# Optimization experiments

Hardware: AMD Instinct MI355X
Metric: run time of the kernel (lower is better)

Reference implementation:

```python
import jax, jax.numpy as jnp
import numpy as np

N = 100000      # num_nodes
E = 400000      # num edges
HID = 128       # hidden_channels (== in_channels, memory dim)
OUT = 64        # out_channels (per head)
HEADS = 4
HD = HEADS * OUT  # 256, TransformerConv concat output dim


def _lin(k, fan_in, fan_out):
    return jax.random.normal(k, (fan_in, fan_out), jnp.float32) * 0.02


def setup_inputs() -> dict:
    key = jax.random.key(0)
    ks = jax.random.split(key, 16)
    return {
        "edge_index": jax.random.randint(ks[0], (2, E), 0, N, dtype=jnp.int64),
        "edge_time": jax.random.randint(ks[1], (E, 1), 0, 1000000, dtype=jnp.int64),
        "x": jax.random.normal(ks[2], (N, HID), jnp.float32),
        "memory": jax.random.normal(ks[3], (N, HID), jnp.float32),  # TGN memory table (detached in fwd)
        # TransformerConv params (lin_query / lin_key / lin_value / lin_skip, all with bias)
        "Wq": _lin(ks[4], HID, HD), "bq": jnp.zeros((HD,), jnp.float32),
        "Wk": _lin(ks[5], HID, HD), "bk": jnp.zeros((HD,), jnp.float32),
        "Wv": _lin(ks[6], HID, HD), "bv": jnp.zeros((HD,), jnp.float32),
        "Wskip": _lin(ks[7], HID, HD), "bskip": jnp.zeros((HD,), jnp.float32),
        # rating MLP: Linear(512,128) -> ReLU -> Linear(128,64) -> ReLU -> Linear(64,1)
        "W1": _lin(ks[8], 2 * HD, 128), "b1": jnp.zeros((128,), jnp.float32),
        "W2": _lin(ks[9], 128, 64), "b2": jnp.zeros((64,), jnp.float32),
        "W3": _lin(ks[10], 64, 1), "b3": jnp.zeros((1,), jnp.float32),
    }


def reference(edge_index, edge_time, x, memory,
              Wq, bq, Wk, bk, Wv, bv, Wskip, bskip,
              W1, b1, W2, b2, W3, b3):
    src, dst = edge_index[0], edge_index[1]
    n = x.shape[0]

    # x = memory.detach() + x
    h = memory + x  # [N, HID]

    # TransformerConv (heads=4, concat=True, root_weight=True)
    q = (h @ Wq + bq).reshape(n, HEADS, OUT)
    k = (h @ Wk + bk).reshape(n, HEADS, OUT)
    v = (h @ Wv + bv).reshape(n, HEADS, OUT)

    # per-edge attention scores: messages flow src -> dst, softmax over in-edges of dst
    scores = jnp.sum(q[dst] * k[src], axis=-1) / jnp.sqrt(jnp.float32(OUT))  # [E, H]
    smax = jax.ops.segment_max(scores, dst, num_segments=n)                   # [N, H]
    e = jnp.exp(scores - smax[dst])
    denom = jax.ops.segment_sum(e, dst, num_segments=n)
    alpha = e / (denom[dst] + 1e-16)                                          # [E, H]

    agg = jax.ops.segment_sum(alpha[:, :, None] * v[src], dst, num_segments=n)  # [N, H, OUT]
    out = agg.reshape(n, HD) + (h @ Wskip + bskip)                              # skip connection

    # interaction embeddings + MLP head (dropout inactive at eval)
    inter = jnp.concatenate([out[src], out[dst]], axis=-1)  # [E, 512]
    hdd = jax.nn.relu(inter @ W1 + b1)
    hdd = jax.nn.relu(hdd @ W2 + b2)
    rating = jax.nn.sigmoid(hdd @ W3 + b3) * 4.0 + 1.0
    return rating[:, 0]
```

## Files before the change

kernel.cpp:

```cpp
#include <hip/hip_runtime.h>
#include <math.h>

#define N_NODES 100000
#define N_EDGES 400000
#define HID 128
#define HEADS 4
#define OUT_C 64
#define HD 256
#define SCAN_CHUNK 1024
#define NB_SCAN ((N_NODES + SCAN_CHUNK - 1) / SCAN_CHUNK)

typedef __attribute__((ext_vector_type(8))) short bf16x8;
typedef __attribute__((ext_vector_type(4))) float f32x4;

__device__ __forceinline__ unsigned short fbf(float f) {
    unsigned u = __float_as_uint(f);
    unsigned r = (u + 0x7fffu + ((u >> 16) & 1u)) >> 16;
    return (unsigned short)r;
}
__device__ __forceinline__ float bf2f(unsigned short u) {
    return __uint_as_float(((unsigned)u) << 16);
}

__global__ __launch_bounds__(256) void init_zero(int* __restrict__ deg,
                                                 int* __restrict__ cursor) {
    int i = blockIdx.x * 256 + threadIdx.x;
    if (i < N_NODES) { deg[i] = 0; cursor[i] = 0; }
}

__global__ __launch_bounds__(256) void k_deg(const int* __restrict__ ei,
                                             int* __restrict__ deg) {
    int e = blockIdx.x * 256 + threadIdx.x;
    if (e < N_EDGES) atomicAdd(&deg[ei[N_EDGES + e]], 1);
}

__global__ __launch_bounds__(256) void k_scan1(const int* __restrict__ deg,
                                               int* __restrict__ rp,
                                               int* __restrict__ bsum) {
    __shared__ int ts[256];
    int b = blockIdx.x, t = threadIdx.x;
    int base = b * SCAN_CHUNK + t * 4;
    int vv[4];
    int s = 0;
#pragma unroll
    for (int i = 0; i < 4; ++i) {
        int d = (base + i < N_NODES) ? deg[base + i] : 0;
        vv[i] = s;
        s += d;
    }
    ts[t] = s;
    __syncthreads();
    for (int off = 1; off < 256; off <<= 1) {
        int x = (t >= off) ? ts[t - off] : 0;
        __syncthreads();
        ts[t] += x;
        __syncthreads();
    }
    int ex = ts[t] - s;
#pragma unroll
    for (int i = 0; i < 4; ++i)
        if (base + i < N_NODES) rp[base + i] = ex + vv[i];
    if (t == 255) bsum[b] = ts[255];
}

__global__ __launch_bounds__(256) void k_scan2(int* __restrict__ bsum) {
    __shared__ int ts[256];
    int t = threadIdx.x;
    int v = (t < NB_SCAN) ? bsum[t] : 0;
    ts[t] = v;
    __syncthreads();
    for (int off = 1; off < 256; off <<= 1) {
        int x = (t >= off) ? ts[t - off] : 0;
        __syncthreads();
        ts[t] += x;
        __syncthreads();
    }
    if (t < NB_SCAN) bsum[t] = ts[t] - v;
}

__global__ __launch_bounds__(256) void k_scan3(int* __restrict__ rp,
                                               const int* __restrict__ bsum) {
    int i = blockIdx.x * 256 + threadIdx.x;
    if (i < N_NODES) rp[i] += bsum[i / SCAN_CHUNK];
}

__global__ __launch_bounds__(256) void k_bucket(const int* __restrict__ ei,
                                                const int* __restrict__ rp,
                                                int* __restrict__ cursor,
                                                int* __restrict__ csr_src,
                                                int* __restrict__ csr_dst,
                                                int* __restrict__ csr_eid) {
    int e = blockIdx.x * 256 + threadIdx.x;
    if (e >= N_EDGES) return;
    int src = ei[e];
    int d   = ei[N_EDGES + e];
    int idx = atomicAdd(&cursor[d], 1);
    int s   = rp[d] + idx;
    csr_src[s] = src;
    csr_dst[s] = d;
    csr_eid[s] = e;
}

__global__ __launch_bounds__(256) void pack_wg(
    const float* __restrict__ Wq, const float* __restrict__ Wk,
    const float* __restrict__ Wv, const float* __restrict__ Ws,
    unsigned short* __restrict__ Wp) {
    int i = blockIdx.x * 256 + threadIdx.x;
    if (i >= 16384) return;
    int lane = i & 63, nt = (i >> 6) & 15, kt = (i >> 10) & 3, z = i >> 12;
    const float* W = (z == 0) ? Wq : (z == 1) ? Wk : (z == 2) ? Wv : Ws;
    int q = lane >> 4, c = lane & 15;
#pragma unroll
    for (int j = 0; j < 8; ++j)
        Wp[i * 8 + j] = fbf(W[(kt * 32 + q * 8 + j) * HD + nt * 16 + c]);
}

__global__ __launch_bounds__(256) void pack_wc(const float* __restrict__ W1,
                                               unsigned short* __restrict__ Wcp) {
    int i = blockIdx.x * 256 + threadIdx.x;
    if (i >= 8192) return;
    int lane = i & 63, nt = (i >> 6) & 15, kt = i >> 10;
    int q = lane >> 4, c = lane & 15;
    int n = nt * 16 + c;
#pragma unroll
    for (int j = 0; j < 8; ++j) {
        int k = kt * 32 + q * 8 + j;
        float v = (n < 128) ? W1[k * 128 + n] : W1[(k + 256) * 128 + (n - 128)];
        Wcp[i * 8 + j] = fbf(v);
    }
}

__global__ __launch_bounds__(256) void pack_w2(const float* __restrict__ W2,
                                               unsigned short* __restrict__ W2p) {
    int i = blockIdx.x * 256 + threadIdx.x;
    if (i >= 1024) return;
    int lane = i & 63, nt = (i >> 6) & 3, kt = i >> 8;
    int q = lane >> 4, c = lane & 15;
#pragma unroll
    for (int j = 0; j < 8; ++j)
        W2p[i * 8 + j] = fbf(W2[(kt * 32 + q * 8 + j) * 64 + nt * 16 + c]);
}

__global__ __launch_bounds__(256) void gemm_proj(
    const float* __restrict__ x, const float* __restrict__ mem,
    const unsigned short* __restrict__ Wp,
    const float* __restrict__ bq, const float* __restrict__ bk,
    const float* __restrict__ bv, const float* __restrict__ bs,
    unsigned short* __restrict__ Q, unsigned short* __restrict__ K,
    unsigned short* __restrict__ V, unsigned short* __restrict__ S)
{
    __shared__ __align__(16) short As[64 * 136];
    __shared__ __align__(16) short Slab[4 * 64 * 68];

    const int t = threadIdx.x;
    const int w = t >> 6, l = t & 63;
    const int q = l >> 4, c = l & 15;
    const int m0 = blockIdx.x * 64;

    {
        const float4* x4 = (const float4*)x;
        const float4* m4 = (const float4*)mem;
#pragma unroll
        for (int j = 0; j < 8; ++j) {
            int idx = t + j * 256;
            int row = idx >> 5, c4 = idx & 31;
            int gr  = m0 + row;
            ushort4 hv = make_ushort4(0, 0, 0, 0);
            if (gr < N_NODES) {
                float4 a = x4[(size_t)gr * 32 + c4];
                float4 b = m4[(size_t)gr * 32 + c4];
                hv = make_ushort4(fbf(a.x + b.x), fbf(a.y + b.y),
                                  fbf(a.z + b.z), fbf(a.w + b.w));
            }
            *(ushort4*)&As[row * 136 + c4 * 4] = hv;
        }
    }
    __syncthreads();

    short* slab = &Slab[w * 64 * 68];
    const int srow = l >> 3;
    const int schk = l & 7;

    for (int z = 0; z < 4; ++z) {
        const float* bz = (z == 0) ? bq : (z == 1) ? bk : (z == 2) ? bv : bs;
        unsigned short* Oz = (z == 0) ? Q : (z == 1) ? K : (z == 2) ? V : S;

        f32x4 acc[4][4];
#pragma unroll
        for (int mt = 0; mt < 4; ++mt)
#pragma unroll
            for (int nt = 0; nt < 4; ++nt) acc[mt][nt] = (f32x4){0.f, 0.f, 0.f, 0.f};

#pragma unroll
        for (int kt = 0; kt < 4; ++kt) {
            bf16x8 af[4];
#pragma unroll
            for (int mt = 0; mt < 4; ++mt)
                af[mt] = *(const bf16x8*)&As[(mt * 16 + c) * 136 + kt * 32 + q * 8];
#pragma unroll
            for (int nt = 0; nt < 4; ++nt) {
                int ntg = w * 4 + nt;
                bf16x8 bv8 = *(const bf16x8*)&Wp[(size_t)(((z * 4 + kt) * 16 + ntg) * 64 + l) * 8];
#pragma unroll
                for (int mt = 0; mt < 4; ++mt)
                    acc[mt][nt] = __builtin_amdgcn_mfma_f32_16x16x32_bf16(af[mt], bv8, acc[mt][nt], 0, 0, 0);
            }
        }

#pragma unroll
        for (int nt = 0; nt < 4; ++nt) {
            float bb = bz[w * 64 + nt * 16 + c];
#pragma unroll
            for (int mt = 0; mt < 4; ++mt)
#pragma unroll
                for (int r = 0; r < 4; ++r)
                    slab[(mt * 16 + q * 4 + r) * 68 + nt * 16 + c] =
                        (short)fbf(acc[mt][nt][r] + bb);
        }
#pragma unroll
        for (int j = 0; j < 8; ++j) {
            int row = j * 8 + srow;
            int gr = m0 + row;
            if (gr < N_NODES)
                *(bf16x8*)&Oz[(size_t)gr * HD + w * 64 + schk * 8] =
                    *(const bf16x8*)&slab[row * 68 + schk * 8];
        }
    }
}

__global__ __launch_bounds__(256) void k_attn(
    const int* __restrict__ rp, const int* __restrict__ deg,
    const int* __restrict__ csr_src,
    const unsigned short* __restrict__ Q, const unsigned short* __restrict__ K,
    const unsigned short* __restrict__ V, const unsigned short* __restrict__ S,
    unsigned short* __restrict__ out)
{
    int node = blockIdx.x * 4 + (threadIdx.x >> 6);
    int l = threadIdx.x & 63;
    if (node >= N_NODES) return;
    int start = rp[node];
    int cnt   = deg[node];

    float q0, q1, q2, q3;
    {
        ushort4 u = *(const ushort4*)&Q[(size_t)node * HD + l * 4];
        q0 = bf2f(u.x); q1 = bf2f(u.y); q2 = bf2f(u.z); q3 = bf2f(u.w);
    }

    float m = -1e30f, d = 0.f;
    float a0 = 0.f, a1 = 0.f, a2 = 0.f, a3 = 0.f;

    for (int i = 0; i < cnt; ++i) {
        int src = csr_src[start + i];
        ushort4 ku = *(const ushort4*)&K[(size_t)src * HD + l * 4];
        float s = q0 * bf2f(ku.x) + q1 * bf2f(ku.y) + q2 * bf2f(ku.z) + q3 * bf2f(ku.w);
        s += __shfl_xor(s, 1);
        s += __shfl_xor(s, 2);
        s += __shfl_xor(s, 4);
        s += __shfl_xor(s, 8);
        s *= 0.125f;

        float mn    = fmaxf(m, s);
        float scale = __expf(m - mn);
        float e     = __expf(s - mn);
        d = d * scale + e;
        ushort4 vu = *(const ushort4*)&V[(size_t)src * HD + l * 4];
        a0 = a0 * scale + e * bf2f(vu.x);
        a1 = a1 * scale + e * bf2f(vu.y);
        a2 = a2 * scale + e * bf2f(vu.z);
        a3 = a3 * scale + e * bf2f(vu.w);
        m = mn;
    }

    float inv = 1.f / (d + 1e-16f);
    ushort4 su = *(const ushort4*)&S[(size_t)node * HD + l * 4];
    ushort4 ov = make_ushort4(fbf(bf2f(su.x) + a0 * inv),
                              fbf(bf2f(su.y) + a1 * inv),
                              fbf(bf2f(su.z) + a2 * inv),
                              fbf(bf2f(su.w) + a3 * inv));
    *(ushort4*)&out[(size_t)node * HD + l * 4] = ov;
}

__global__ __launch_bounds__(256) void pd_gemm(
    const unsigned short* __restrict__ outb,
    const unsigned short* __restrict__ Wcp,
    unsigned short* __restrict__ PD)
{
    __shared__ __align__(16) char sh[4 * 64 * 68 * 2];
    short* As   = (short*)sh;
    short* Slab = (short*)sh;

    const int t = threadIdx.x;
    const int w = t >> 6, l = t & 63;
    const int q = l >> 4, c = l & 15;
    const int m0 = blockIdx.x * 64;

#pragma unroll
    for (int j = 0; j < 8; ++j) {
        int idx = t + j * 256;
        int row = idx >> 5, c4 = idx & 31;
        int gr  = m0 + row;
        bf16x8 v = (bf16x8){0,0,0,0,0,0,0,0};
        if (gr < N_NODES)
            v = *(const bf16x8*)&outb[(size_t)gr * HD + c4 * 8];
        *(bf16x8*)&As[row * 264 + c4 * 8] = v;
    }
    __syncthreads();

    f32x4 acc[4][4];
#pragma unroll
    for (int mt = 0; mt < 4; ++mt)
#pragma unroll
        for (int nt = 0; nt < 4; ++nt) acc[mt][nt] = (f32x4){0.f, 0.f, 0.f, 0.f};

#pragma unroll
    for (int kt = 0; kt < 8; ++kt) {
        bf16x8 af[4];
#pragma unroll
        for (int mt = 0; mt < 4; ++mt)
            af[mt] = *(const bf16x8*)&As[(mt * 16 + c) * 264 + kt * 32 + q * 8];
#pragma unroll
        for (int nt = 0; nt < 4; ++nt) {
            int ntg = w * 4 + nt;
            bf16x8 bv8 = *(const bf16x8*)&Wcp[(size_t)((kt * 16 + ntg) * 64 + l) * 8];
#pragma unroll
            for (int mt = 0; mt < 4; ++mt)
                acc[mt][nt] = __builtin_amdgcn_mfma_f32_16x16x32_bf16(af[mt], bv8, acc[mt][nt], 0, 0, 0);
        }
    }
    __syncthreads();

    short* slab = &Slab[w * 64 * 68];
#pragma unroll
    for (int nt = 0; nt < 4; ++nt)
#pragma unroll
        for (int mt = 0; mt < 4; ++mt)
#pragma unroll
            for (int r = 0; r < 4; ++r)
                slab[(mt * 16 + q * 4 + r) * 68 + nt * 16 + c] =
                    (short)fbf(acc[mt][nt][r]);
    const int srow = l >> 3, schk = l & 7;
#pragma unroll
    for (int j = 0; j < 8; ++j) {
        int row = j * 8 + srow;
        int gr = m0 + row;
        if (gr < N_NODES)
            *(bf16x8*)&PD[(size_t)gr * HD + w * 64 + schk * 8] =
                *(const bf16x8*)&slab[row * 68 + schk * 8];
    }
}

__global__ __launch_bounds__(256) void edge_mlp_pd(
    const int* __restrict__ csr_src, const int* __restrict__ csr_dst,
    const int* __restrict__ csr_eid,
    const unsigned short* __restrict__ PD,
    const float* __restrict__ b1,
    const unsigned short* __restrict__ W2p, const float* __restrict__ b2,
    const float* __restrict__ W3, const float* __restrict__ b3,
    float* __restrict__ rating)
{
    __shared__ __align__(16) char lds[64 * 136 * 2];
    short* h1t = (short*)lds;
    float* h2s = (float*)lds;

    const int t = threadIdx.x;
    const int w = t >> 6, l = t & 63;
    const int q = l >> 4, c = l & 15;
    const int e0 = blockIdx.x * 64;

#pragma unroll
    for (int j = 0; j < 4; ++j) {
        int idx = t + j * 256;
        int row = idx >> 4, ch = idx & 15;
        int src = csr_src[e0 + row];
        int dst = csr_dst[e0 + row];
        bf16x8 pv = *(const bf16x8*)&PD[(size_t)src * HD + ch * 8];
        bf16x8 dv = *(const bf16x8*)&PD[(size_t)dst * HD + 128 + ch * 8];
        float4 ba = *(const float4*)&b1[ch * 8];
        float4 bb = *(const float4*)&b1[ch * 8 + 4];
        bf16x8 hv;
        hv[0] = (short)fbf(fmaxf(bf2f((unsigned short)pv[0]) + bf2f((unsigned short)dv[0]) + ba.x, 0.f));
        hv[1] = (short)fbf(fmaxf(bf2f((unsigned short)pv[1]) + bf2f((unsigned short)dv[1]) + ba.y, 0.f));
        hv[2] = (short)fbf(fmaxf(bf2f((unsigned short)pv[2]) + bf2f((unsigned short)dv[2]) + ba.z, 0.f));
        hv[3] = (short)fbf(fmaxf(bf2f((unsigned short)pv[3]) + bf2f((unsigned short)dv[3]) + ba.w, 0.f));
        hv[4] = (short)fbf(fmaxf(bf2f((unsigned short)pv[4]) + bf2f((unsigned short)dv[4]) + bb.x, 0.f));
        hv[5] = (short)fbf(fmaxf(bf2f((unsigned short)pv[5]) + bf2f((unsigned short)dv[5]) + bb.y, 0.f));
        hv[6] = (short)fbf(fmaxf(bf2f((unsigned short)pv[6]) + bf2f((unsigned short)dv[6]) + bb.z, 0.f));
        hv[7] = (short)fbf(fmaxf(bf2f((unsigned short)pv[7]) + bf2f((unsigned short)dv[7]) + bb.w, 0.f));
        *(bf16x8*)&h1t[row * 136 + ch * 8] = hv;
    }
    __syncthreads();

    f32x4 acc2[4];
#pragma unroll
    for (int i = 0; i < 4; ++i) acc2[i] = (f32x4){0.f, 0.f, 0.f, 0.f};
#pragma unroll
    for (int kt = 0; kt < 4; ++kt) {
        bf16x8 av = *(const bf16x8*)&h1t[(w * 16 + c) * 136 + kt * 32 + q * 8];
#pragma unroll
        for (int nt = 0; nt < 4; ++nt) {
            bf16x8 bv = *(const bf16x8*)&W2p[(size_t)((kt * 4 + nt) * 64 + l) * 8];
            acc2[nt] = __builtin_amdgcn_mfma_f32_16x16x32_bf16(av, bv, acc2[nt], 0, 0, 0);
        }
    }
    __syncthreads();

#pragma unroll
    for (int nt = 0; nt < 4; ++nt) {
        float bv = b2[nt * 16 + c];
#pragma unroll
        for (int r = 0; r < 4; ++r)
            h2s[(w * 16 + q * 4 + r) * 65 + nt * 16 + c] = fmaxf(acc2[nt][r] + bv, 0.f);
    }
    __syncthreads();

    if (t < 64) {
        float a = b3[0];
#pragma unroll 8
        for (int kk = 0; kk < 64; ++kk)
            a += h2s[t * 65 + kk] * W3[kk];
        rating[csr_eid[e0 + t]] = 4.f / (1.f + __expf(-a)) + 1.f;
    }
}

extern "C" void kernel_launch(void* const* d_in, const int* in_sizes, int n_in,
                              void* d_out, int out_size, void* d_ws, size_t ws_size,
                              hipStream_t stream) {
    const int*   ei  = (const int*)d_in[0];
    const float* x   = (const float*)d_in[2];
    const float* mem = (const float*)d_in[3];
    const float* Wq  = (const float*)d_in[4];
    const float* bq  = (const float*)d_in[5];
    const float* Wk  = (const float*)d_in[6];
    const float* bk  = (const float*)d_in[7];
    const float* Wv  = (const float*)d_in[8];
    const float* bv  = (const float*)d_in[9];
    const float* Ws  = (const float*)d_in[10];
    const float* bs  = (const float*)d_in[11];
    const float* W1  = (const float*)d_in[12];
    const float* b1  = (const float*)d_in[13];
    const float* W2  = (const float*)d_in[14];
    const float* b2  = (const float*)d_in[15];
    const float* W3  = (const float*)d_in[16];
    const float* b3  = (const float*)d_in[17];
    float* rating = (float*)d_out;

    unsigned short* Q = (unsigned short*)d_ws;
    const size_t NHDe = (size_t)N_NODES * HD;
    unsigned short* K = Q + NHDe;
    unsigned short* V = K + NHDe;
    unsigned short* S = V + NHDe;
    int* rp      = (int*)(S + NHDe);
    int* deg     = rp + N_NODES;
    int* cursor  = deg + N_NODES;
    int* csr_src = cursor + N_NODES;
    int* csr_dst = csr_src + N_EDGES;
    int* csr_eid = csr_dst + N_EDGES;
    int* bsum    = csr_eid + N_EDGES;
    unsigned short* Wp  = (unsigned short*)(bsum + 128);
    unsigned short* Wcp = Wp + 16384 * 8;
    unsigned short* W2p = Wcp + 8192 * 8;
    unsigned short* PD  = K;

    const int nblk  = (N_NODES + 255) / 256;
    const int eblk  = (N_EDGES + 255) / 256;
    const int wgrid = (N_NODES + 3) / 4;

    init_zero<<<nblk, 256, 0, stream>>>(deg, cursor);
    k_deg<<<eblk, 256, 0, stream>>>(ei, deg);
    k_scan1<<<NB_SCAN, 256, 0, stream>>>(deg, rp, bsum);
    k_scan2<<<1, 256, 0, stream>>>(bsum);
    k_scan3<<<nblk, 256, 0, stream>>>(rp, bsum);
    k_bucket<<<eblk, 256, 0, stream>>>(ei, rp, cursor, csr_src, csr_dst, csr_eid);
    pack_wg<<<64, 256, 0, stream>>>(Wq, Wk, Wv, Ws, Wp);
    pack_wc<<<32, 256, 0, stream>>>(W1, Wcp);
    pack_w2<<<4, 256, 0, stream>>>(W2, W2p);

    gemm_proj<<<(N_NODES + 63) / 64, 256, 0, stream>>>(
        x, mem, Wp, bq, bk, bv, bs, Q, K, V, S);

    k_attn<<<wgrid, 256, 0, stream>>>(rp, deg, csr_src, Q, K, V, S, Q);

    pd_gemm<<<(N_NODES + 63) / 64, 256, 0, stream>>>(Q, Wcp, PD);

    edge_mlp_pd<<<N_EDGES / 64, 256, 0, stream>>>(
        csr_src, csr_dst, csr_eid, PD, b1, W2p, b2, W3, b3, rating);
}
```

Before: 500.3 us.

## Interleave K and V rows, split projection GEMM over grid, precompute bf16 H

Adds a pre-pass that converts memory+x to a bf16 H table. The projection GEMM is split across a 2D grid with one output matrix per blockIdx.y, and it loads H tiles straight into LDS with XOR-swizzled global_load_lds. K and V are stored interleaved in one 512-wide row, so the attention gather fetches both from the same row region. This buys more parallelism and better locality for the per-edge gather. The cost is an extra kernel launch, an extra round trip of H through memory, and each A tile being reloaded four times.

```diff
diff --git a/kernel.cpp b/kernel.cpp
--- a/kernel.cpp
+++ b/kernel.cpp
@@ -20,6 +20,13 @@
 }
 __device__ __forceinline__ float bf2f(unsigned short u) {
     return __uint_as_float(((unsigned)u) << 16);
+}
+
+__device__ __forceinline__ void gl_lds16(const void* g, void* l) {
+    __builtin_amdgcn_global_load_lds(
+        (const __attribute__((address_space(1))) unsigned int*)g,
+        (__attribute__((address_space(3))) unsigned int*)l,
+        16, 0, 0);
 }
 
 __global__ __launch_bounds__(256) void init_zero(int* __restrict__ deg,
@@ -141,98 +148,111 @@
         W2p[i * 8 + j] = fbf(W2[(kt * 32 + q * 8 + j) * 64 + nt * 16 + c]);
 }
 
-__global__ __launch_bounds__(256) void gemm_proj(
-    const float* __restrict__ x, const float* __restrict__ mem,
+__global__ __launch_bounds__(256) void k_pre(const float* __restrict__ x,
+                                             const float* __restrict__ mem,
+                                             unsigned short* __restrict__ H) {
+    int idx = blockIdx.x * 256 + threadIdx.x;
+    if (idx >= N_NODES * HID / 8) return;
+    const float4* x4 = (const float4*)x;
+    const float4* m4 = (const float4*)mem;
+    float4 a0 = x4[(size_t)idx * 2],     a1 = x4[(size_t)idx * 2 + 1];
+    float4 b0 = m4[(size_t)idx * 2],     b1 = m4[(size_t)idx * 2 + 1];
+    bf16x8 hv;
+    hv[0] = (short)fbf(a0.x + b0.x); hv[1] = (short)fbf(a0.y + b0.y);
+    hv[2] = (short)fbf(a0.z + b0.z); hv[3] = (short)fbf(a0.w + b0.w);
+    hv[4] = (short)fbf(a1.x + b1.x); hv[5] = (short)fbf(a1.y + b1.y);
+    hv[6] = (short)fbf(a1.z + b1.z); hv[7] = (short)fbf(a1.w + b1.w);
+    *(bf16x8*)&H[(size_t)idx * 8] = hv;
+}
+
+__global__ __launch_bounds__(256, 4) void gemm4(
+    const unsigned short* __restrict__ H,
     const unsigned short* __restrict__ Wp,
     const float* __restrict__ bq, const float* __restrict__ bk,
     const float* __restrict__ bv, const float* __restrict__ bs,
-    unsigned short* __restrict__ Q, unsigned short* __restrict__ K,
-    unsigned short* __restrict__ V, unsigned short* __restrict__ S)
+    unsigned short* __restrict__ Q, unsigned short* __restrict__ KV,
+    unsigned short* __restrict__ S)
 {
-    __shared__ __align__(16) short As[64 * 136];
-    __shared__ __align__(16) short Slab[4 * 64 * 68];
+    __shared__ __align__(16) short sh[4 * 64 * 68];
+    short* As = sh;
 
     const int t = threadIdx.x;
     const int w = t >> 6, l = t & 63;
     const int q = l >> 4, c = l & 15;
+    const int z  = blockIdx.y;
     const int m0 = blockIdx.x * 64;
 
-    {
-        const float4* x4 = (const float4*)x;
-        const float4* m4 = (const float4*)mem;
-#pragma unroll
-        for (int j = 0; j < 8; ++j) {
-            int idx = t + j * 256;
-            int row = idx >> 5, c4 = idx & 31;
-            int gr  = m0 + row;
-            ushort4 hv = make_ushort4(0, 0, 0, 0);
-            if (gr < N_NODES) {
-                float4 a = x4[(size_t)gr * 32 + c4];
-                float4 b = m4[(size_t)gr * 32 + c4];
-                hv = make_ushort4(fbf(a.x + b.x), fbf(a.y + b.y),
-                                  fbf(a.z + b.z), fbf(a.w + b.w));
-            }
-            *(ushort4*)&As[row * 136 + c4 * 4] = hv;
+#pragma unroll
+    for (int i = 0; i < 4; ++i) {
+        int rbase = w * 16 + i * 4;
+        int r  = rbase + (l >> 4);
+        int gr = m0 + r; if (gr >= N_NODES) gr = N_NODES - 1;
+        int ks = (l & 15) ^ (r & 7);
+        gl_lds16(&H[(size_t)gr * HID + ks * 8], &As[rbase * 128]);
+    }
+
+    unsigned short* Oz; int rs, coff; const float* bz;
+    if      (z == 0) { Oz = Q;  rs = 256; coff = 0;   bz = bq; }
+    else if (z == 1) { Oz = KV; rs = 512; coff = 0;   bz = bk; }
+    else if (z == 2) { Oz = KV; rs = 512; coff = 256; bz = bv; }
+    else             { Oz = S;  rs = 256; coff = 0;   bz = bs; }
+    float bb[4];
+#pragma unroll
+    for (int nt = 0; nt < 4; ++nt) bb[nt] = bz[w * 64 + nt * 16 + c];
+
+    f32x4 acc[4][4];
+#pragma unroll
+    for (int mt = 0; mt < 4; ++mt)
+#pragma unroll
+        for (int nt = 0; nt < 4; ++nt) acc[mt][nt] = (f32x4){0.f, 0.f, 0.f, 0.f};
+
+    __syncthreads();
+
+#pragma unroll
+    for (int kt = 0; kt < 4; ++kt) {
+        bf16x8 af[4];
+#pragma unroll
+        for (int mt = 0; mt < 4; ++mt) {
+            int row  = mt * 16 + c;
+            int slot = (kt * 4 + q) ^ (row & 7);
+            af[mt] = *(const bf16x8*)&As[row * 128 + slot * 8];
         }
-    }
-    __syncthreads();
-
-    short* slab = &Slab[w * 64 * 68];
-    const int srow = l >> 3;
-    const int schk = l & 7;
-
-    for (int z = 0; z < 4; ++z) {
-        const float* bz = (z == 0) ? bq : (z == 1) ? bk : (z == 2) ? bv : bs;
-        unsigned short* Oz = (z == 0) ? Q : (z == 1) ? K : (z == 2) ? V : S;
-
-        f32x4 acc[4][4];
+#pragma unroll
+        for (int nt = 0; nt < 4; ++nt) {
+            bf16x8 bw8 = *(const bf16x8*)&Wp[(size_t)(((z * 4 + kt) * 16 + w * 4 + nt) * 64 + l) * 8];
+#pragma unroll
+            for (int mt = 0; mt < 4; ++mt)
+                acc[mt][nt] = __builtin_amdgcn_mfma_f32_16x16x32_bf16(af[mt], bw8, acc[mt][nt], 0, 0, 0);
+        }
+    }
+    __syncthreads();
+
+    short* slab = &sh[w * 64 * 68];
+#pragma unroll
+    for (int nt = 0; nt < 4; ++nt)
 #pragma unroll
         for (int mt = 0; mt < 4; ++mt)
 #pragma unroll
-            for (int nt = 0; nt < 4; ++nt) acc[mt][nt] = (f32x4){0.f, 0.f, 0.f, 0.f};
-
-#pragma unroll
-        for (int kt = 0; kt < 4; ++kt) {
-            bf16x8 af[4];
-#pragma unroll
-            for (int mt = 0; mt < 4; ++mt)
-                af[mt] = *(const bf16x8*)&As[(mt * 16 + c) * 136 + kt * 32 + q * 8];
-#pragma unroll
-            for (int nt = 0; nt < 4; ++nt) {
-                int ntg = w * 4 + nt;
-                bf16x8 bv8 = *(const bf16x8*)&Wp[(size_t)(((z * 4 + kt) * 16 + ntg) * 64 + l) * 8];
-#pragma unroll
-                for (int mt = 0; mt < 4; ++mt)
-                    acc[mt][nt] = __builtin_amdgcn_mfma_f32_16x16x32_bf16(af[mt], bv8, acc[mt][nt], 0, 0, 0);
-            }
-        }
-
-#pragma unroll
-        for (int nt = 0; nt < 4; ++nt) {
-            float bb = bz[w * 64 + nt * 16 + c];
-#pragma unroll
-            for (int mt = 0; mt < 4; ++mt)
-#pragma unroll
-                for (int r = 0; r < 4; ++r)
-                    slab[(mt * 16 + q * 4 + r) * 68 + nt * 16 + c] =
-                        (short)fbf(acc[mt][nt][r] + bb);
-        }
-#pragma unroll
-        for (int j = 0; j < 8; ++j) {
-            int row = j * 8 + srow;
-            int gr = m0 + row;
-            if (gr < N_NODES)
-                *(bf16x8*)&Oz[(size_t)gr * HD + w * 64 + schk * 8] =
-                    *(const bf16x8*)&slab[row * 68 + schk * 8];
-        }
+            for (int r = 0; r < 4; ++r)
+                slab[(mt * 16 + q * 4 + r) * 68 + nt * 16 + c] =
+                    (short)fbf(acc[mt][nt][r] + bb[nt]);
+
+    const int srow = l >> 3, schk = l & 7;
+#pragma unroll
+    for (int j = 0; j < 8; ++j) {
+        int row = j * 8 + srow;
+        int gr  = m0 + row;
+        if (gr < N_NODES)
+            *(bf16x8*)&Oz[(size_t)gr * rs + coff + w * 64 + schk * 8] =
+                *(const bf16x8*)&slab[row * 68 + schk * 8];
     }
 }
 
 __global__ __launch_bounds__(256) void k_attn(
     const int* __restrict__ rp, const int* __restrict__ deg,
     const int* __restrict__ csr_src,
-    const unsigned short* __restrict__ Q, const unsigned short* __restrict__ K,
-    const unsigned short* __restrict__ V, const unsigned short* __restrict__ S,
+    const unsigned short* __restrict__ Q, const unsigned short* __restrict__ KV,
+    const unsigned short* __restrict__ S,
     unsigned short* __restrict__ out)
 {
     int node = blockIdx.x * 4 + (threadIdx.x >> 6);
@@ -252,7 +272,9 @@
 
     for (int i = 0; i < cnt; ++i) {
         int src = csr_src[start + i];
-        ushort4 ku = *(const ushort4*)&K[(size_t)src * HD + l * 4];
+        const unsigned short* kv = &KV[(size_t)src * 512 + l * 4];
+        ushort4 ku = *(const ushort4*)kv;
+        ushort4 vu = *(const ushort4*)(kv + 256);
         float s = q0 * bf2f(ku.x) + q1 * bf2f(ku.y) + q2 * bf2f(ku.z) + q3 * bf2f(ku.w);
         s += __shfl_xor(s, 1);
         s += __shfl_xor(s, 2);
@@ -264,7 +286,6 @@
         float scale = __expf(m - mn);
         float e     = __expf(s - mn);
         d = d * scale + e;
-        ushort4 vu = *(const ushort4*)&V[(size_t)src * HD + l * 4];
         a0 = a0 * scale + e * bf2f(vu.x);
         a1 = a1 * scale + e * bf2f(vu.y);
         a2 = a2 * scale + e * bf2f(vu.z);
@@ -447,10 +468,10 @@
 
     unsigned short* Q = (unsigned short*)d_ws;
     const size_t NHDe = (size_t)N_NODES * HD;
-    unsigned short* K = Q + NHDe;
-    unsigned short* V = K + NHDe;
-    unsigned short* S = V + NHDe;
-    int* rp      = (int*)(S + NHDe);
+    unsigned short* KV = Q + NHDe;
+    unsigned short* S  = KV + 2 * NHDe;
+    unsigned short* H  = S + NHDe;
+    int* rp      = (int*)(H + (size_t)N_NODES * HID);
     int* deg     = rp + N_NODES;
     int* cursor  = deg + N_NODES;
     int* csr_src = cursor + N_NODES;
@@ -460,11 +481,12 @@
     unsigned short* Wp  = (unsigned short*)(bsum + 128);
     unsigned short* Wcp = Wp + 16384 * 8;
     unsigned short* W2p = Wcp + 8192 * 8;
-    unsigned short* PD  = K;
+    unsigned short* PD  = KV;
 
     const int nblk  = (N_NODES + 255) / 256;
     const int eblk  = (N_EDGES + 255) / 256;
     const int wgrid = (N_NODES + 3) / 4;
+    const int pblk  = (N_NODES * HID / 8 + 255) / 256;
 
     init_zero<<<nblk, 256, 0, stream>>>(deg, cursor);
     k_deg<<<eblk, 256, 0, stream>>>(ei, deg);
@@ -476,10 +498,12 @@
     pack_wc<<<32, 256, 0, stream>>>(W1, Wcp);
     pack_w2<<<4, 256, 0, stream>>>(W2, W2p);
 
-    gemm_proj<<<(N_NODES + 63) / 64, 256, 0, stream>>>(
-        x, mem, Wp, bq, bk, bv, bs, Q, K, V, S);
-
-    k_attn<<<wgrid, 256, 0, stream>>>(rp, deg, csr_src, Q, K, V, S, Q);
+    k_pre<<<pblk, 256, 0, stream>>>(x, mem, H);
+
+    gemm4<<<dim3((N_NODES + 63) / 64, 4), dim3(256), 0, stream>>>(
+        H, Wp, bq, bk, bv, bs, Q, KV, S);
+
+    k_attn<<<wgrid, 256, 0, stream>>>(rp, deg, csr_src, Q, KV, S, Q);
 
     pd_gemm<<<(N_NODES + 63) / 64, 256, 0, stream>>>(Q, Wcp, PD);
 
```

New measurement: 429.8 us. -14.1%, faster.
